# Performance work log

Hardware: AMD Instinct MI355X
Metric: run time of the kernel (lower is better)

Reference implementation:

```python
import jax, jax.numpy as jnp
import numpy as np

NEG_INF = -1e25


def setup_inputs() -> dict:
    key = jax.random.key(0)
    ks = jax.random.split(key, 7)
    B, L, Q, H = 4, 512, 64, 768
    bert = jax.random.normal(ks[0], (B, L, H), dtype=jnp.float32)
    query = jax.random.normal(ks[1], (B, Q, H), dtype=jnp.float32)
    mask = jax.random.randint(ks[2], (B, L), 0, 2).astype(bool)
    # nn.Linear(2H, H): weight (H, 2H), bias (H)
    W_w = jax.random.normal(ks[3], (H, 2 * H), dtype=jnp.float32) * (1.0 / np.sqrt(2 * H))
    W_b = jax.random.normal(ks[4], (H,), dtype=jnp.float32) * 0.02
    # nn.Linear(H, 1): weight (1, H), bias (1)
    v_w = jax.random.normal(ks[5], (1, H), dtype=jnp.float32) * (1.0 / np.sqrt(H))
    v_b = jax.random.normal(ks[6], (1,), dtype=jnp.float32) * 0.02
    return {"bert": bert, "query": query, "mask": mask,
            "W_w": W_w, "W_b": W_b, "v_w": v_w, "v_b": v_b}


def reference(bert, query, mask, W_w, W_b, v_w, v_b):
    H = bert.shape[-1]
    # Linear(cat([bert, query])) = bert @ Wb^T + query @ Wq^T + b  (avoids the (B,Q,L,2H) concat)
    W_bert = W_w[:, :H]    # (H, H) acts on bert part
    W_query = W_w[:, H:]   # (H, H) acts on query part
    bp = jnp.einsum('blh,kh->blk', bert, W_bert)     # (B, L, H)
    qp = jnp.einsum('bqh,kh->bqk', query, W_query)   # (B, Q, H)
    h = jnp.tanh(bp[:, None, :, :] + qp[:, :, None, :] + W_b)  # (B, Q, L, H)
    x = jnp.einsum('bqlh,h->bql', h, v_w[0]) + v_b[0]           # (B, Q, L)
    x = jnp.where(mask[:, None, :], x, NEG_INF)
    return jax.nn.softmax(x, axis=-1)
```

## Files before the change

kernel.cpp:

```cpp
#include <hip/hip_runtime.h>
#include <hip/hip_bf16.h>

#define LOG2E    1.4426950408889634f
#define TWOLOG2E 2.8853900817779268f

typedef short bf16x8 __attribute__((ext_vector_type(8)));
typedef float f32x4  __attribute__((ext_vector_type(4)));
typedef unsigned short u16x8 __attribute__((ext_vector_type(8)));

static __device__ __forceinline__ float bf16_to_f(unsigned short u) {
    union { unsigned int i; float f; } v; v.i = ((unsigned int)u) << 16; return v.f;
}
static __device__ __forceinline__ unsigned short f_to_bf16_rne(float x) {
    union { float f; unsigned int i; } v; v.f = x;
    unsigned int lsb = (v.i >> 16) & 1u;
    v.i += 0x7fffu + lsb;
    return (unsigned short)(v.i >> 16);
}

__global__ __launch_bounds__(256) void cast_frag(
    const float* __restrict__ bert, const float* __restrict__ query,
    const float* __restrict__ Ww,
    unsigned short* __restrict__ Ahf, unsigned short* __restrict__ Alf,
    unsigned short* __restrict__ Whf, unsigned short* __restrict__ Wlf)
{
    const int i    = blockIdx.x * 256 + threadIdx.x;
    const int lane = i & 63;
    const float* src;
    float scale;
    unsigned short *dh, *dl;
    size_t di;
    if (i < 221184) {
        const int rest = i >> 6;
        const int kt = rest % 24, mt = rest / 24;
        const int m  = mt * 16 + (lane & 15);
        src = ((m < 2048) ? bert + (size_t)m * 768
                          : query + (size_t)(m - 2048) * 768)
              + kt * 32 + (lane >> 4) * 8;
        scale = 1.0f;
        dh = Ahf; dl = Alf; di = (size_t)i * 8;
    } else {
        const int j = i - 221184;
        const int rest = j >> 6;
        const int kt = rest % 24, nt2 = rest / 24;
        const int sel = (nt2 >= 48) ? 1 : 0;
        const int n   = (nt2 - sel * 48) * 16 + (lane & 15);
        src = Ww + (size_t)n * 1536 + sel * 768 + kt * 32 + (lane >> 4) * 8;
        scale = TWOLOG2E;
        dh = Whf; dl = Wlf; di = (size_t)j * 8;
    }
    float4 x0 = *(const float4*)src;
    float4 x1 = *(const float4*)(src + 4);
    float xs[8] = {x0.x * scale, x0.y * scale, x0.z * scale, x0.w * scale,
                   x1.x * scale, x1.y * scale, x1.z * scale, x1.w * scale};
    u16x8 h, l;
    #pragma unroll
    for (int e = 0; e < 8; ++e) {
        unsigned short hh = f_to_bf16_rne(xs[e]);
        h[e] = hh;
        l[e] = f_to_bf16_rne(xs[e] - bf16_to_f(hh));
    }
    *(u16x8*)(dh + di) = h;
    *(u16x8*)(dl + di) = l;
}

__global__ __launch_bounds__(64) void gemm_frag(
    const unsigned short* __restrict__ Ahf, const unsigned short* __restrict__ Alf,
    const unsigned short* __restrict__ Whf, const unsigned short* __restrict__ Wlf,
    const float* __restrict__ Wb, float* __restrict__ C)
{
    const int l    = threadIdx.x;
    const int w    = blockIdx.x;
    const int mt_w = w / 24;
    const int nt_w = w % 24;
    const int m0   = mt_w * 32;
    const int n0   = nt_w * 32;
    const bool isq = (m0 >= 2048);
    const int  fmt = mt_w * 2;
    const int  fnt = (isq ? 48 : 0) + nt_w * 2;
    const int  lr  = l & 15;
    const int  kg  = l >> 4;

    const unsigned short* pAh = Ahf + (size_t)fmt * 12288 + l * 8;
    const unsigned short* pAl = Alf + (size_t)fmt * 12288 + l * 8;
    const unsigned short* pBh = Whf + (size_t)fnt * 12288 + l * 8;
    const unsigned short* pBl = Wlf + (size_t)fnt * 12288 + l * 8;

    f32x4 acc[2][2];
    #pragma unroll
    for (int i = 0; i < 2; ++i)
        #pragma unroll
        for (int j = 0; j < 2; ++j) acc[i][j] = (f32x4){0.f, 0.f, 0.f, 0.f};

    #pragma unroll 4
    for (int kt = 0; kt < 24; ++kt) {
        bf16x8 ah[2], al[2], bh[2], bl[2];
        #pragma unroll
        for (int i = 0; i < 2; ++i) {
            ah[i] = *(const bf16x8*)(pAh + (size_t)i * 12288 + kt * 512);
            al[i] = *(const bf16x8*)(pAl + (size_t)i * 12288 + kt * 512);
            bh[i] = *(const bf16x8*)(pBh + (size_t)i * 12288 + kt * 512);
            bl[i] = *(const bf16x8*)(pBl + (size_t)i * 12288 + kt * 512);
        }
        #pragma unroll
        for (int i = 0; i < 2; ++i)
            #pragma unroll
            for (int j = 0; j < 2; ++j) {
                acc[i][j] = __builtin_amdgcn_mfma_f32_16x16x32_bf16(ah[i], bh[j], acc[i][j], 0, 0, 0);
                acc[i][j] = __builtin_amdgcn_mfma_f32_16x16x32_bf16(ah[i], bl[j], acc[i][j], 0, 0, 0);
                acc[i][j] = __builtin_amdgcn_mfma_f32_16x16x32_bf16(al[i], bh[j], acc[i][j], 0, 0, 0);
            }
    }

    #pragma unroll
    for (int j = 0; j < 2; ++j) {
        const int col  = n0 + j * 16 + lr;
        const float bias = isq ? Wb[col] * TWOLOG2E : 0.f;
        #pragma unroll
        for (int i = 0; i < 2; ++i)
            #pragma unroll
            for (int r = 0; r < 4; ++r) {
                const int row = m0 + i * 16 + kg * 4 + r;
                C[(size_t)row * 768 + col] = acc[i][j][r] + bias;
            }
    }
}

__global__ __launch_bounds__(256) void attn_scores_part(
    const float* __restrict__ C, const float* __restrict__ v_w,
    float* __restrict__ Xp)
{
    const int t  = threadIdx.x;
    const int bz = blockIdx.z;
    const int b  = bz >> 2;
    const int ks = bz & 3;
    const int q  = blockIdx.y * 16 + (t >> 4);
    const int lx = blockIdx.x * 16 + (t & 15);
    const int k0 = ks * 192;
    const float* pb = C + (size_t)(b * 512 + lx) * 768 + k0;
    const float* pq = C + (size_t)(2048 + b * 64 + q) * 768 + k0;
    const float* pv = v_w + k0;
    float acc = 0.f;
    #pragma unroll 4
    for (int k = 0; k < 192; k += 4) {
        float4 bv = *(const float4*)(pb + k);
        float4 qv = *(const float4*)(pq + k);
        float4 vv = *(const float4*)(pv + k);
        acc = fmaf(vv.x, __builtin_amdgcn_rcpf(1.0f + __builtin_amdgcn_exp2f(bv.x + qv.x)), acc);
        acc = fmaf(vv.y, __builtin_amdgcn_rcpf(1.0f + __builtin_amdgcn_exp2f(bv.y + qv.y)), acc);
        acc = fmaf(vv.z, __builtin_amdgcn_rcpf(1.0f + __builtin_amdgcn_exp2f(bv.z + qv.z)), acc);
        acc = fmaf(vv.w, __builtin_amdgcn_rcpf(1.0f + __builtin_amdgcn_exp2f(bv.w + qv.w)), acc);
    }
    Xp[(size_t)ks * 131072 + (size_t)(b * 64 + q) * 512 + lx] = acc;
}

__global__ __launch_bounds__(512) void softmax_mask(
    const float* __restrict__ Xp, const int* __restrict__ mask,
    float* __restrict__ out)
{
    const int bq  = blockIdx.x;
    const int b   = bq >> 6;
    const int l   = threadIdx.x;
    const int wid = l >> 6;
    __shared__ float red[8];

    const size_t idx = (size_t)bq * 512 + l;
    float v = -2.f * (Xp[idx] + Xp[idx + 131072] + Xp[idx + 262144] + Xp[idx + 393216]);
    const bool mk = (mask[b * 512 + l] != 0);
    v = mk ? v : -1e25f;

    float m = v;
    #pragma unroll
    for (int o = 32; o; o >>= 1) m = fmaxf(m, __shfl_xor(m, o));
    if ((l & 63) == 0) red[wid] = m;
    __syncthreads();
    #pragma unroll
    for (int i = 0; i < 8; ++i) m = fmaxf(m, red[i]);

    float e = __builtin_amdgcn_exp2f((v - m) * LOG2E);
    float s = e;
    #pragma unroll
    for (int o = 32; o; o >>= 1) s += __shfl_xor(s, o);
    __syncthreads();
    if ((l & 63) == 0) red[wid] = s;
    __syncthreads();
    s = 0.f;
    #pragma unroll
    for (int i = 0; i < 8; ++i) s += red[i];

    out[idx] = e / s;
}

extern "C" void kernel_launch(void* const* d_in, const int* in_sizes, int n_in,
                              void* d_out, int out_size, void* d_ws, size_t ws_size,
                              hipStream_t stream)
{
    const float* bert  = (const float*)d_in[0];
    const float* query = (const float*)d_in[1];
    const int*   mask  = (const int*)  d_in[2];
    const float* W_w   = (const float*)d_in[3];
    const float* W_b   = (const float*)d_in[4];
    const float* v_w   = (const float*)d_in[5];
    const float* v_b   = (const float*)d_in[6];
    (void)v_b;

    float* C  = (float*)d_ws;
    float* Xp = C + (size_t)2304 * 768;
    unsigned short* Ahf = (unsigned short*)(Xp + (size_t)4 * 256 * 512);
    unsigned short* Alf = Ahf + (size_t)2304 * 768;
    unsigned short* Whf = Alf + (size_t)2304 * 768;
    unsigned short* Wlf = Whf + (size_t)1536 * 768;
    float* out = (float*)d_out;

    cast_frag<<<1440, 256, 0, stream>>>(bert, query, W_w, Ahf, Alf, Whf, Wlf);
    gemm_frag<<<1728, 64, 0, stream>>>(Ahf, Alf, Whf, Wlf, W_b, C);
    attn_scores_part<<<dim3(32, 4, 16), 256, 0, stream>>>(C, v_w, Xp);
    softmax_mask<<<dim3(256), 512, 0, stream>>>(Xp, mask, out);
}
```

Measured before the change: 148.3 us.

## Store bert projection transposed and restructure score kernel for coalesced loads

The GEMM now writes the bert projection transposed (H x B*L) by swapping MFMA operand roles, and writes the query projection to a separate buffer. The score kernel is rewritten so each block handles one (b,q) row over a 96-wide K slice, with each thread reading coalesced float4 columns of the transposed bert projection and broadcasting scalar q and v values. The K split goes from 4 to 8 partials, and softmax sums 8 partial buffers. This is meant to replace redundant per-thread strided row reads with coalesced loads and scalar broadcasts, at the cost of more partial-sum traffic.

Result: faster. 130.4 us (-12.1%).

```diff
diff --git a/kernel.cpp b/kernel.cpp
--- a/kernel.cpp
+++ b/kernel.cpp
@@ -67,7 +67,7 @@
 __global__ __launch_bounds__(64) void gemm_frag(
     const unsigned short* __restrict__ Ahf, const unsigned short* __restrict__ Alf,
     const unsigned short* __restrict__ Whf, const unsigned short* __restrict__ Wlf,
-    const float* __restrict__ Wb, float* __restrict__ C)
+    const float* __restrict__ Wb, float* __restrict__ bpT, float* __restrict__ qp)
 {
     const int l    = threadIdx.x;
     const int w    = blockIdx.x;
@@ -92,66 +92,94 @@
         #pragma unroll
         for (int j = 0; j < 2; ++j) acc[i][j] = (f32x4){0.f, 0.f, 0.f, 0.f};
 
-    #pragma unroll 4
-    for (int kt = 0; kt < 24; ++kt) {
-        bf16x8 ah[2], al[2], bh[2], bl[2];
-        #pragma unroll
-        for (int i = 0; i < 2; ++i) {
-            ah[i] = *(const bf16x8*)(pAh + (size_t)i * 12288 + kt * 512);
-            al[i] = *(const bf16x8*)(pAl + (size_t)i * 12288 + kt * 512);
-            bh[i] = *(const bf16x8*)(pBh + (size_t)i * 12288 + kt * 512);
-            bl[i] = *(const bf16x8*)(pBl + (size_t)i * 12288 + kt * 512);
+    if (!isq) {
+        #pragma unroll 4
+        for (int kt = 0; kt < 24; ++kt) {
+            bf16x8 ah[2], al[2], bh[2], bl[2];
+            #pragma unroll
+            for (int i = 0; i < 2; ++i) {
+                ah[i] = *(const bf16x8*)(pAh + (size_t)i * 12288 + kt * 512);
+                al[i] = *(const bf16x8*)(pAl + (size_t)i * 12288 + kt * 512);
+                bh[i] = *(const bf16x8*)(pBh + (size_t)i * 12288 + kt * 512);
+                bl[i] = *(const bf16x8*)(pBl + (size_t)i * 12288 + kt * 512);
+            }
+            #pragma unroll
+            for (int i = 0; i < 2; ++i)
+                #pragma unroll
+                for (int j = 0; j < 2; ++j) {
+                    acc[i][j] = __builtin_amdgcn_mfma_f32_16x16x32_bf16(bh[i], ah[j], acc[i][j], 0, 0, 0);
+                    acc[i][j] = __builtin_amdgcn_mfma_f32_16x16x32_bf16(bh[i], al[j], acc[i][j], 0, 0, 0);
+                    acc[i][j] = __builtin_amdgcn_mfma_f32_16x16x32_bf16(bl[i], ah[j], acc[i][j], 0, 0, 0);
+                }
         }
         #pragma unroll
         for (int i = 0; i < 2; ++i)
             #pragma unroll
-            for (int j = 0; j < 2; ++j) {
-                acc[i][j] = __builtin_amdgcn_mfma_f32_16x16x32_bf16(ah[i], bh[j], acc[i][j], 0, 0, 0);
-                acc[i][j] = __builtin_amdgcn_mfma_f32_16x16x32_bf16(ah[i], bl[j], acc[i][j], 0, 0, 0);
-                acc[i][j] = __builtin_amdgcn_mfma_f32_16x16x32_bf16(al[i], bh[j], acc[i][j], 0, 0, 0);
+            for (int j = 0; j < 2; ++j)
+                #pragma unroll
+                for (int r = 0; r < 4; ++r) {
+                    const int nrow = n0 + i * 16 + kg * 4 + r;
+                    const int mcol = m0 + j * 16 + lr;
+                    bpT[(size_t)nrow * 2048 + mcol] = acc[i][j][r];
+                }
+    } else {
+        #pragma unroll 4
+        for (int kt = 0; kt < 24; ++kt) {
+            bf16x8 ah[2], al[2], bh[2], bl[2];
+            #pragma unroll
+            for (int i = 0; i < 2; ++i) {
+                ah[i] = *(const bf16x8*)(pAh + (size_t)i * 12288 + kt * 512);
+                al[i] = *(const bf16x8*)(pAl + (size_t)i * 12288 + kt * 512);
+                bh[i] = *(const bf16x8*)(pBh + (size_t)i * 12288 + kt * 512);
+                bl[i] = *(const bf16x8*)(pBl + (size_t)i * 12288 + kt * 512);
             }
-    }
-
-    #pragma unroll
-    for (int j = 0; j < 2; ++j) {
-        const int col  = n0 + j * 16 + lr;
-        const float bias = isq ? Wb[col] * TWOLOG2E : 0.f;
+            #pragma unroll
+            for (int i = 0; i < 2; ++i)
+                #pragma unroll
+                for (int j = 0; j < 2; ++j) {
+                    acc[i][j] = __builtin_amdgcn_mfma_f32_16x16x32_bf16(ah[i], bh[j], acc[i][j], 0, 0, 0);
+                    acc[i][j] = __builtin_amdgcn_mfma_f32_16x16x32_bf16(ah[i], bl[j], acc[i][j], 0, 0, 0);
+                    acc[i][j] = __builtin_amdgcn_mfma_f32_16x16x32_bf16(al[i], bh[j], acc[i][j], 0, 0, 0);
+                }
+        }
         #pragma unroll
-        for (int i = 0; i < 2; ++i)
-            #pragma unroll
-            for (int r = 0; r < 4; ++r) {
-                const int row = m0 + i * 16 + kg * 4 + r;
-                C[(size_t)row * 768 + col] = acc[i][j][r] + bias;
-            }
-    }
-}
-
-__global__ __launch_bounds__(256) void attn_scores_part(
-    const float* __restrict__ C, const float* __restrict__ v_w,
-    float* __restrict__ Xp)
+        for (int j = 0; j < 2; ++j) {
+            const int col  = n0 + j * 16 + lr;
+            const float bias = Wb[col] * TWOLOG2E;
+            #pragma unroll
+            for (int i = 0; i < 2; ++i)
+                #pragma unroll
+                for (int r = 0; r < 4; ++r) {
+                    const int row = m0 - 2048 + i * 16 + kg * 4 + r;
+                    qp[(size_t)row * 768 + col] = acc[i][j][r] + bias;
+                }
+        }
+    }
+}
+
+__global__ __launch_bounds__(128) void attn_dense(
+    const float* __restrict__ bpT, const float* __restrict__ qp,
+    const float* __restrict__ v_w, float* __restrict__ Xp)
 {
     const int t  = threadIdx.x;
-    const int bz = blockIdx.z;
-    const int b  = bz >> 2;
-    const int ks = bz & 3;
-    const int q  = blockIdx.y * 16 + (t >> 4);
-    const int lx = blockIdx.x * 16 + (t & 15);
-    const int k0 = ks * 192;
-    const float* pb = C + (size_t)(b * 512 + lx) * 768 + k0;
-    const float* pq = C + (size_t)(2048 + b * 64 + q) * 768 + k0;
-    const float* pv = v_w + k0;
-    float acc = 0.f;
+    const int bq = blockIdx.x;
+    const int ks = blockIdx.y;
+    const int b  = bq >> 6;
+    const int k0 = ks * 96;
+    const float* bT = bpT + (size_t)b * 512 + t * 4;
+    const float* pq = qp + (size_t)bq * 768;
+    f32x4 acc = {0.f, 0.f, 0.f, 0.f};
     #pragma unroll 4
-    for (int k = 0; k < 192; k += 4) {
-        float4 bv = *(const float4*)(pb + k);
-        float4 qv = *(const float4*)(pq + k);
-        float4 vv = *(const float4*)(pv + k);
-        acc = fmaf(vv.x, __builtin_amdgcn_rcpf(1.0f + __builtin_amdgcn_exp2f(bv.x + qv.x)), acc);
-        acc = fmaf(vv.y, __builtin_amdgcn_rcpf(1.0f + __builtin_amdgcn_exp2f(bv.y + qv.y)), acc);
-        acc = fmaf(vv.z, __builtin_amdgcn_rcpf(1.0f + __builtin_amdgcn_exp2f(bv.z + qv.z)), acc);
-        acc = fmaf(vv.w, __builtin_amdgcn_rcpf(1.0f + __builtin_amdgcn_exp2f(bv.w + qv.w)), acc);
-    }
-    Xp[(size_t)ks * 131072 + (size_t)(b * 64 + q) * 512 + lx] = acc;
+    for (int k = k0; k < k0 + 96; ++k) {
+        float4 bv = *(const float4*)(bT + (size_t)k * 2048);
+        const float qk = pq[k];
+        const float vk = v_w[k];
+        acc[0] = fmaf(vk, __builtin_amdgcn_rcpf(1.0f + __builtin_amdgcn_exp2f(bv.x + qk)), acc[0]);
+        acc[1] = fmaf(vk, __builtin_amdgcn_rcpf(1.0f + __builtin_amdgcn_exp2f(bv.y + qk)), acc[1]);
+        acc[2] = fmaf(vk, __builtin_amdgcn_rcpf(1.0f + __builtin_amdgcn_exp2f(bv.z + qk)), acc[2]);
+        acc[3] = fmaf(vk, __builtin_amdgcn_rcpf(1.0f + __builtin_amdgcn_exp2f(bv.w + qk)), acc[3]);
+    }
+    *(f32x4*)(Xp + (size_t)ks * 131072 + (size_t)bq * 512 + t * 4) = acc;
 }
 
 __global__ __launch_bounds__(512) void softmax_mask(
@@ -165,7 +193,10 @@
     __shared__ float red[8];
 
     const size_t idx = (size_t)bq * 512 + l;
-    float v = -2.f * (Xp[idx] + Xp[idx + 131072] + Xp[idx + 262144] + Xp[idx + 393216]);
+    float v = 0.f;
+    #pragma unroll
+    for (int p = 0; p < 8; ++p) v += Xp[idx + (size_t)p * 131072];
+    v *= -2.f;
     const bool mk = (mask[b * 512 + l] != 0);
     v = mk ? v : -1e25f;
 
@@ -204,16 +235,17 @@
     const float* v_b   = (const float*)d_in[6];
     (void)v_b;
 
-    float* C  = (float*)d_ws;
-    float* Xp = C + (size_t)2304 * 768;
-    unsigned short* Ahf = (unsigned short*)(Xp + (size_t)4 * 256 * 512);
+    float* bpT = (float*)d_ws;
+    float* qp  = bpT + (size_t)768 * 2048;
+    float* Xp  = qp  + (size_t)256 * 768;
+    unsigned short* Ahf = (unsigned short*)(Xp + (size_t)8 * 256 * 512);
     unsigned short* Alf = Ahf + (size_t)2304 * 768;
     unsigned short* Whf = Alf + (size_t)2304 * 768;
     unsigned short* Wlf = Whf + (size_t)1536 * 768;
     float* out = (float*)d_out;
 
     cast_frag<<<1440, 256, 0, stream>>>(bert, query, W_w, Ahf, Alf, Whf, Wlf);
-    gemm_frag<<<1728, 64, 0, stream>>>(Ahf, Alf, Whf, Wlf, W_b, C);
-    attn_scores_part<<<dim3(32, 4, 16), 256, 0, stream>>>(C, v_w, Xp);
+    gemm_frag<<<1728, 64, 0, stream>>>(Ahf, Alf, Whf, Wlf, W_b, bpT, qp);
+    attn_dense<<<dim3(256, 8), 128, 0, stream>>>(bpT, qp, v_w, Xp);
     softmax_mask<<<dim3(256), 512, 0, stream>>>(Xp, mask, out);
 }
```
